# Optimization experiments

Hardware: AMD Instinct MI355X
Metric: run time of the kernel (lower is better)

The kernel has to match this reference:

```python
import jax, jax.numpy as jnp
import numpy as np

B, S, HID = 2, 1024, 2048
HQ, HKV, HD = 32, 8, 64
ROPE_BASE = 10000.0

def _rope_tables(seq_len, head_dim):
    inv_freq = 1.0 / (ROPE_BASE ** (np.arange(0, head_dim, 2, dtype=np.float32) / head_dim))
    t = np.arange(seq_len, dtype=np.float32)
    freqs = np.outer(t, inv_freq)                      # [S, d/2]
    emb = np.concatenate([freqs, freqs], axis=-1)      # [S, d]
    return jnp.asarray(np.cos(emb)), jnp.asarray(np.sin(emb))

def setup_inputs() -> dict:
    key = jax.random.key(0)
    ks = jax.random.split(key, 5)
    cos, sin = _rope_tables(S, HD)
    return {
        'hidden_states': jax.random.normal(ks[0], (B, S, HID), jnp.float32),
        'cos': cos, 'sin': sin,
        'Wq': jax.random.normal(ks[1], (HID, HID), jnp.float32) * (HID ** -0.5),
        'Wk': jax.random.normal(ks[2], (HID, HKV * HD), jnp.float32) * (HID ** -0.5),
        'Wv': jax.random.normal(ks[3], (HID, HKV * HD), jnp.float32) * (HID ** -0.5),
        'Wo': jax.random.normal(ks[4], (HID, HID), jnp.float32) * (HID ** -0.5),
    }

def _rotate_half(x):
    d = x.shape[-1]
    return jnp.concatenate([-x[..., d // 2:], x[..., :d // 2]], axis=-1)

def reference(hidden_states, cos, sin, Wq, Wk, Wv, Wo):
    b, s, _ = hidden_states.shape
    q = (hidden_states @ Wq).reshape(b, s, HQ, HD)    # [b,s,Hq,d]
    k = (hidden_states @ Wk).reshape(b, s, HKV, HD)   # [b,s,Hkv,d]
    v = (hidden_states @ Wv).reshape(b, s, HKV, HD)
    # RoPE: cos/sin [s,d] broadcast as [s,1,d] over head dim
    c = cos[:, None, :]
    sn = sin[:, None, :]
    q = q * c + _rotate_half(q) * sn
    k = k * c + _rotate_half(k) * sn
    # GQA: expand kv heads to query heads (repeat_kv)
    n_rep = HQ // HKV
    k = jnp.repeat(k, n_rep, axis=2)                  # [b,s,Hq,d]
    v = jnp.repeat(v, n_rep, axis=2)
    scale = HD ** -0.5
    scores = jnp.einsum('bqhd,bkhd->bhqk', q, k) * scale  # [b,Hq,s,s]
    causal = jnp.tril(jnp.ones((s, s), bool))
    scores = jnp.where(causal, scores, jnp.float32(-1e30))
    probs = jax.nn.softmax(scores.astype(jnp.float32), axis=-1).astype(q.dtype)
    out = jnp.einsum('bhqk,bkhd->bqhd', probs, v).reshape(b, s, HID)
    return out @ Wo
```

## Files before the change

### kernel.cpp

```cpp
#include <hip/hip_runtime.h>
#include <math.h>

#define B_   2
#define S_   1024
#define HID_ 2048
#define HQ_  32
#define HKV_ 8
#define HD_  64
#define NQKV 3072

#define PCHUNK 2097152

using short8  = __attribute__((ext_vector_type(8))) short;
using floatx4 = __attribute__((ext_vector_type(4))) float;

__device__ __forceinline__ unsigned short f2bf(float x) {
    unsigned int u = __builtin_bit_cast(unsigned int, x);
    u += 0x7FFFu + ((u >> 16) & 1u);
    return (unsigned short)(u >> 16);
}
__device__ __forceinline__ float bf2f(unsigned short u) {
    return __builtin_bit_cast(float, (unsigned int)u << 16);
}

__device__ __forceinline__ void gl_lds16(const unsigned short* g, unsigned short* l) {
    __builtin_amdgcn_global_load_lds(
        (const __attribute__((address_space(1))) void*)g,
        (__attribute__((address_space(3))) void*)l, 16, 0, 0);
}

__global__ __launch_bounds__(256) void gemm_qkv(const unsigned short* __restrict__ A,
                                                const unsigned short* __restrict__ Bt,
                                                unsigned short* __restrict__ Qp,
                                                unsigned short* __restrict__ KVp) {
    __shared__ __align__(16) unsigned short As[128 * 64];
    __shared__ __align__(16) unsigned short Bs[128 * 64];

    int bid = blockIdx.x;
    int m0, n0, z, Nw, nc0;
    unsigned short* C;
    if (bid < 512) {
        n0 = (bid & 15) * 128; m0 = ((bid >> 4) & 15) * 128; z = bid >> 8;
        C = Qp + (size_t)z * 2048 * 2048; Nw = 2048; nc0 = n0;
    } else {
        bid -= 512;
        n0 = 2048 + (bid & 7) * 128; m0 = ((bid >> 3) & 15) * 128; z = bid >> 7;
        C = KVp + (size_t)z * 2048 * 1024; Nw = 1024; nc0 = n0 - 2048;
    }
    const int kbase = z * 1024;

    const int tid  = threadIdx.x;
    const int w    = tid >> 6;
    const int lane = tid & 63;
    const int col  = lane & 15;
    const int quad = lane >> 4;
    const int wm = (w >> 1) * 64;
    const int wn = (w & 1) * 64;

    const int srow = lane >> 3;
    const int scol = ((lane & 7) ^ srow) * 8;
    const unsigned short* Ag = A  + (size_t)(m0 + w * 32 + srow) * HID_ + scol;
    const unsigned short* Bg = Bt + (size_t)(n0 + w * 32 + srow) * HID_ + scol;

    floatx4 acc[4][4] = {};

    for (int k0 = kbase; k0 < kbase + 1024; k0 += 64) {
#pragma unroll
        for (int c = 0; c < 4; ++c) {
            gl_lds16(Ag + (size_t)(8 * c) * HID_ + k0, &As[(w * 32 + 8 * c) * 64]);
            gl_lds16(Bg + (size_t)(8 * c) * HID_ + k0, &Bs[(w * 32 + 8 * c) * 64]);
        }
        __syncthreads();

#pragma unroll
        for (int hh = 0; hh < 2; ++hh) {
            short8 af[4], bfr[4];
#pragma unroll
            for (int i = 0; i < 4; ++i)
                af[i] = *(const short8*)&As[(wm + i * 16 + col) * 64
                                            + (((hh * 4 + quad) ^ (col & 7)) << 3)];
#pragma unroll
            for (int j = 0; j < 4; ++j)
                bfr[j] = *(const short8*)&Bs[(wn + j * 16 + col) * 64
                                             + (((hh * 4 + quad) ^ (col & 7)) << 3)];
#pragma unroll
            for (int i = 0; i < 4; ++i)
#pragma unroll
                for (int j = 0; j < 4; ++j)
                    acc[i][j] = __builtin_amdgcn_mfma_f32_16x16x32_bf16(
                        af[i], bfr[j], acc[i][j], 0, 0, 0);
        }
        __syncthreads();
    }

#pragma unroll
    for (int i = 0; i < 4; ++i)
#pragma unroll
        for (int j = 0; j < 4; ++j)
#pragma unroll
            for (int r = 0; r < 4; ++r)
                C[(size_t)(m0 + wm + i * 16 + quad * 4 + r) * Nw
                  + (nc0 + wn + j * 16 + col)] = f2bf(acc[i][j][r]);
}

__global__ __launch_bounds__(256) void gemm_wo(const unsigned short* __restrict__ A,
                                               const unsigned short* __restrict__ Bt,
                                               float* __restrict__ Cf,
                                               unsigned short* __restrict__ Cp1) {
    __shared__ __align__(16) unsigned short As[128 * 64];
    __shared__ __align__(16) unsigned short Bs[128 * 64];

    const int m0 = blockIdx.y * 128;
    const int n0 = blockIdx.x * 128;
    const int z  = blockIdx.z;
    const int kbase = z * 1024;

    const int tid  = threadIdx.x;
    const int w    = tid >> 6;
    const int lane = tid & 63;
    const int col  = lane & 15;
    const int quad = lane >> 4;
    const int wm = (w >> 1) * 64;
    const int wn = (w & 1) * 64;

    const int srow = lane >> 3;
    const int scol = ((lane & 7) ^ srow) * 8;
    const unsigned short* Ag = A  + (size_t)(m0 + w * 32 + srow) * HID_ + scol;
    const unsigned short* Bg = Bt + (size_t)(n0 + w * 32 + srow) * HID_ + scol;

    floatx4 acc[4][4] = {};

    for (int k0 = kbase; k0 < kbase + 1024; k0 += 64) {
#pragma unroll
        for (int c = 0; c < 4; ++c) {
            gl_lds16(Ag + (size_t)(8 * c) * HID_ + k0, &As[(w * 32 + 8 * c) * 64]);
            gl_lds16(Bg + (size_t)(8 * c) * HID_ + k0, &Bs[(w * 32 + 8 * c) * 64]);
        }
        __syncthreads();

#pragma unroll
        for (int hh = 0; hh < 2; ++hh) {
            short8 af[4], bfr[4];
#pragma unroll
            for (int i = 0; i < 4; ++i)
                af[i] = *(const short8*)&As[(wm + i * 16 + col) * 64
                                            + (((hh * 4 + quad) ^ (col & 7)) << 3)];
#pragma unroll
            for (int j = 0; j < 4; ++j)
                bfr[j] = *(const short8*)&Bs[(wn + j * 16 + col) * 64
                                             + (((hh * 4 + quad) ^ (col & 7)) << 3)];
#pragma unroll
            for (int i = 0; i < 4; ++i)
#pragma unroll
                for (int j = 0; j < 4; ++j)
                    acc[i][j] = __builtin_amdgcn_mfma_f32_16x16x32_bf16(
                        af[i], bfr[j], acc[i][j], 0, 0, 0);
        }
        __syncthreads();
    }

#pragma unroll
    for (int i = 0; i < 4; ++i)
#pragma unroll
        for (int j = 0; j < 4; ++j)
#pragma unroll
            for (int r = 0; r < 4; ++r) {
                size_t off = (size_t)(m0 + wm + i * 16 + quad * 4 + r) * HID_
                           + (n0 + wn + j * 16 + col);
                if (z == 0) Cf[off] = acc[i][j][r];
                else        Cp1[off] = f2bf(acc[i][j][r]);
            }
}

__global__ __launch_bounds__(256) void reduce_wo(float* __restrict__ out,
                                                 const unsigned short* __restrict__ p1) {
    int i4 = (blockIdx.x * 256 + threadIdx.x) * 4;
    float4 o = *(float4*)&out[i4];
    ushort4 p = *(const ushort4*)&p1[i4];
    o.x += bf2f(p.x); o.y += bf2f(p.y); o.z += bf2f(p.z); o.w += bf2f(p.w);
    *(float4*)&out[i4] = o;
}

__global__ __launch_bounds__(256) void prep(const float* __restrict__ X,
                                            const float* __restrict__ Wq,
                                            const float* __restrict__ Wk,
                                            const float* __restrict__ Wv,
                                            const float* __restrict__ Wo,
                                            unsigned short* __restrict__ Xbf,
                                            unsigned short* __restrict__ WcatT,
                                            unsigned short* __restrict__ WoT) {
    __shared__ float tile[32][33];
    int bid = blockIdx.x;
    if (bid < 4096) {
        int tid = bid * 256 + threadIdx.x;
        float4 v = *(const float4*)&X[(size_t)tid * 4];
        ushort4 o = {f2bf(v.x), f2bf(v.y), f2bf(v.z), f2bf(v.w)};
        *(ushort4*)&Xbf[(size_t)tid * 4] = o;
        return;
    }
    const float* W;
    unsigned short* WT;
    int N, tn0, tk0;
    if (bid < 10240) {
        bid -= 4096;
        if (bid < 4096) {
            W = Wq; WT = WcatT; N = HID_;
            tn0 = (bid & 63) * 32; tk0 = (bid >> 6) * 32;
        } else if (bid < 5120) {
            bid -= 4096;
            W = Wk; WT = WcatT + (size_t)HID_ * HID_; N = 512;
            tn0 = (bid & 15) * 32; tk0 = (bid >> 4) * 32;
        } else {
            bid -= 5120;
            W = Wv; WT = WcatT + (size_t)(HID_ + 512) * HID_; N = 512;
            tn0 = (bid & 15) * 32; tk0 = (bid >> 4) * 32;
        }
    } else {
        bid -= 10240;
        W = Wo; WT = WoT; N = HID_;
        tn0 = (bid & 63) * 32; tk0 = (bid >> 6) * 32;
    }
    const int r  = threadIdx.x >> 3;
    const int c4 = (threadIdx.x & 7) * 4;
    float4 v = *(const float4*)&W[(size_t)(tk0 + r) * N + tn0 + c4];
    tile[r][c4 + 0] = v.x;
    tile[r][c4 + 1] = v.y;
    tile[r][c4 + 2] = v.z;
    tile[r][c4 + 3] = v.w;
    __syncthreads();
    ushort4 o = {f2bf(tile[c4 + 0][r]), f2bf(tile[c4 + 1][r]),
                 f2bf(tile[c4 + 2][r]), f2bf(tile[c4 + 3][r])};
    *(ushort4*)&WT[(size_t)(tn0 + r) * HID_ + tk0 + c4] = o;
}

__global__ __launch_bounds__(256) void transpose_wo(const float* __restrict__ Wo,
                                                    unsigned short* __restrict__ WoT) {
    __shared__ float tile[32][33];
    int bid = blockIdx.x;
    const int tn0 = (bid & 63) * 32;
    const int tk0 = (bid >> 6) * 32;
    const int r  = threadIdx.x >> 3;
    const int c4 = (threadIdx.x & 7) * 4;
    float4 v = *(const float4*)&Wo[(size_t)(tk0 + r) * HID_ + tn0 + c4];
    tile[r][c4 + 0] = v.x;
    tile[r][c4 + 1] = v.y;
    tile[r][c4 + 2] = v.z;
    tile[r][c4 + 3] = v.w;
    __syncthreads();
    ushort4 o = {f2bf(tile[c4 + 0][r]), f2bf(tile[c4 + 1][r]),
                 f2bf(tile[c4 + 2][r]), f2bf(tile[c4 + 3][r])};
    *(ushort4*)&WoT[(size_t)(tn0 + r) * HID_ + tk0 + c4] = o;
}

__global__ __launch_bounds__(256) void convert_qkv(const unsigned short* __restrict__ Qp,
                                                   const unsigned short* __restrict__ KVp,
                                                   const float* __restrict__ cosT,
                                                   const float* __restrict__ sinT,
                                                   unsigned short* __restrict__ Qbf,
                                                   unsigned short* __restrict__ Kbf,
                                                   unsigned short* __restrict__ Vt) {
    const size_t QSTR  = (size_t)2048 * 2048;
    const size_t KVSTR = (size_t)2048 * 1024;
    int tid = blockIdx.x * 256 + threadIdx.x;
    const int NQ4 = 524288;
    const int NK4 = 131072;
    if (tid < NQ4) {
        int d0 = (tid & 7) * 4;
        int h  = (tid >> 3) & 31;
        int s  = (tid >> 8) & 1023;
        int b  = tid >> 18;
        const unsigned short* row = Qp + (size_t)(b * S_ + s) * 2048 + h * HD_;
        ushort4 a0 = *(const ushort4*)&row[d0];
        ushort4 a1 = *(const ushort4*)&row[d0 + 32];
        ushort4 p0 = *(const ushort4*)&row[QSTR + d0];
        ushort4 p1 = *(const ushort4*)&row[QSTR + d0 + 32];
        float4 c0  = *(const float4*)&cosT[s * HD_ + d0];
        float4 sn0 = *(const float4*)&sinT[s * HD_ + d0];
        float4 c1  = *(const float4*)&cosT[s * HD_ + d0 + 32];
        float4 sn1 = *(const float4*)&sinT[s * HD_ + d0 + 32];
        ushort4 o0, o1;
#pragma unroll
        for (int j = 0; j < 4; ++j) {
            float x0 = bf2f(((const unsigned short*)&a0)[j]) +
                       bf2f(((const unsigned short*)&p0)[j]);
            float x1 = bf2f(((const unsigned short*)&a1)[j]) +
                       bf2f(((const unsigned short*)&p1)[j]);
            ((unsigned short*)&o0)[j] =
                f2bf((x0 * ((const float*)&c0)[j] - x1 * ((const float*)&sn0)[j]) * 0.125f);
            ((unsigned short*)&o1)[j] =
                f2bf((x1 * ((const float*)&c1)[j] + x0 * ((const float*)&sn1)[j]) * 0.125f);
        }
        unsigned short* orow = Qbf + ((size_t)(b * HQ_ + h) * S_ + s) * HD_;
        *(ushort4*)&orow[d0]      = o0;
        *(ushort4*)&orow[d0 + 32] = o1;
    } else if (tid < NQ4 + NK4) {
        tid -= NQ4;
        int d0 = (tid & 7) * 4;
        int kv = (tid >> 3) & 7;
        int s  = (tid >> 6) & 1023;
        int b  = tid >> 16;
        const unsigned short* row = KVp + (size_t)(b * S_ + s) * 1024 + kv * HD_;
        ushort4 a0 = *(const ushort4*)&row[d0];
        ushort4 a1 = *(const ushort4*)&row[d0 + 32];
        ushort4 p0 = *(const ushort4*)&row[KVSTR + d0];
        ushort4 p1 = *(const ushort4*)&row[KVSTR + d0 + 32];
        float4 c0  = *(const float4*)&cosT[s * HD_ + d0];
        float4 sn0 = *(const float4*)&sinT[s * HD_ + d0];
        float4 c1  = *(const float4*)&cosT[s * HD_ + d0 + 32];
        float4 sn1 = *(const float4*)&sinT[s * HD_ + d0 + 32];
        ushort4 o0, o1;
#pragma unroll
        for (int j = 0; j < 4; ++j) {
            float x0 = bf2f(((const unsigned short*)&a0)[j]) +
                       bf2f(((const unsigned short*)&p0)[j]);
            float x1 = bf2f(((const unsigned short*)&a1)[j]) +
                       bf2f(((const unsigned short*)&p1)[j]);
            ((unsigned short*)&o0)[j] =
                f2bf(x0 * ((const float*)&c0)[j] - x1 * ((const float*)&sn0)[j]);
            ((unsigned short*)&o1)[j] =
                f2bf(x1 * ((const float*)&c1)[j] + x0 * ((const float*)&sn1)[j]);
        }
        unsigned short* orow = Kbf + ((size_t)(b * HKV_ + kv) * S_ + s) * HD_;
        *(ushort4*)&orow[d0]      = o0;
        *(ushort4*)&orow[d0 + 32] = o1;
    } else {
        tid -= NQ4 + NK4;
        int s4 = tid & 255;
        int d  = (tid >> 8) & (HD_ - 1);
        int kv = (tid >> 14) & (HKV_ - 1);
        int b  = tid >> 17;
        int s  = s4 * 4;
        const unsigned short* base =
            KVp + ((size_t)(b * S_ + s)) * 1024 + 512 + kv * HD_ + d;
        ushort4 o;
#pragma unroll
        for (int j = 0; j < 4; ++j) {
            float v = bf2f(base[(size_t)j * 1024]) +
                      bf2f(base[KVSTR + (size_t)j * 1024]);
            ((unsigned short*)&o)[j] = f2bf(v);
        }
        *(ushort4*)&Vt[((size_t)(b * HKV_ + kv) * HD_ + d) * S_ + s] = o;
    }
}

__global__ __launch_bounds__(256) void attn_mfma(const unsigned short* __restrict__ Qbf,
                                                 const unsigned short* __restrict__ Kbf,
                                                 const unsigned short* __restrict__ Vt,
                                                 unsigned short* __restrict__ Ctx,
                                                 float* __restrict__ PO,
                                                 float* __restrict__ ML) {
    const int x  = blockIdx.x;
    const int kv = blockIdx.y;
    const int b  = blockIdx.z;

    int tq, chunk, it0, it1;
    if (x < 32) {
        tq = 16 + (x >> 1); chunk = x & 1;
        const int ns = (32 * tq + 95) >> 6;
        const int hh = ns >> 1;
        it0 = chunk ? hh : 0;
        it1 = chunk ? ns : hh;
    } else {
        tq = 47 - x; chunk = -1;
        it0 = 0;
        it1 = (32 * tq + 95) >> 6;
    }

    const int w    = threadIdx.x >> 6;
    const int lane = threadIdx.x & 63;
    const int col  = lane & 15;
    const int quad = lane >> 4;

    const int h   = kv * 4 + w;
    const int bh  = b * HQ_ + h;
    const int bkv = b * HKV_ + kv;
    const int qw  = 32 * tq;

    __shared__ __align__(16) unsigned short sK[2][64 * 64];
    __shared__ __align__(16) unsigned short sV[2][64 * 64];
    __shared__ __align__(16) unsigned short sP[4][16 * 64];
    unsigned short* myP = sP[w];

    short8 bq[2][2];
#pragma unroll
    for (int u = 0; u < 2; ++u) {
        const unsigned short* qrow = Qbf + ((size_t)bh * S_ + qw + 16 * u + col) * HD_;
        bq[u][0] = *(const short8*)&qrow[quad * 8];
        bq[u][1] = *(const short8*)&qrow[32 + quad * 8];
    }

    const unsigned short* Kbase = Kbf + (size_t)bkv * S_ * HD_;
    const unsigned short* Vbase = Vt  + (size_t)bkv * HD_ * S_;

    const int sr  = lane >> 3;
    const int ssl = (lane & 7) ^ sr;
    const int r0  = 16 * w;

    floatx4 acc[2][4] = {};
    float m_i[2] = {-1e30f, -1e30f};
    float l_i[2] = {0.f, 0.f};

    {
        const int kb = it0 * 64;
#pragma unroll
        for (int c = 0; c < 2; ++c) {
            const int row = r0 + 8 * c + sr;
            gl_lds16(Kbase + (size_t)(kb + row) * HD_ + ssl * 8, &sK[0][(r0 + 8 * c) * 64]);
            gl_lds16(Vbase + (size_t)row * S_ + kb + ssl * 8,    &sV[0][(r0 + 8 * c) * 64]);
        }
    }
    __syncthreads();

    int cur = 0;
    for (int it = it0; it < it1; ++it) {
        const int k0 = it * 64;

        if (it + 1 < it1) {
            const int kn = k0 + 64;
#pragma unroll
            for (int c = 0; c < 2; ++c) {
                const int row = r0 + 8 * c + sr;
                gl_lds16(Kbase + (size_t)(kn + row) * HD_ + ssl * 8,
                         &sK[cur ^ 1][(r0 + 8 * c) * 64]);
                gl_lds16(Vbase + (size_t)row * S_ + kn + ssl * 8,
                         &sV[cur ^ 1][(r0 + 8 * c) * 64]);
            }
        }

        floatx4 sc[2][4];
        __builtin_amdgcn_s_setprio(1);
#pragma unroll
        for (int tt = 0; tt < 4; ++tt) {
            const int krow = 16 * tt + col;
            const unsigned short* kr = &sK[cur][krow * 64];
            short8 ak0 = *(const short8*)&kr[((quad    ) ^ (krow & 7)) * 8];
            short8 ak1 = *(const short8*)&kr[((quad + 4) ^ (krow & 7)) * 8];
#pragma unroll
            for (int u = 0; u < 2; ++u) {
                floatx4 z = {0.f, 0.f, 0.f, 0.f};
                z = __builtin_amdgcn_mfma_f32_16x16x32_bf16(ak0, bq[u][0], z, 0, 0, 0);
                z = __builtin_amdgcn_mfma_f32_16x16x32_bf16(ak1, bq[u][1], z, 0, 0, 0);
                sc[u][tt] = z;
            }
        }
        __builtin_amdgcn_s_setprio(0);

        short8 pa[2][2];
#pragma unroll
        for (int u = 0; u < 2; ++u) {
            const int qbase = qw + 16 * u;
            const int myq   = qbase + col;
            if (k0 + 63 > qbase) {
#pragma unroll
                for (int tt = 0; tt < 4; ++tt)
#pragma unroll
                    for (int r = 0; r < 4; ++r)
                        if (k0 + 16 * tt + quad * 4 + r > myq) sc[u][tt][r] = -1e30f;
            }
            float vmax = sc[u][0][0];
#pragma unroll
            for (int tt = 0; tt < 4; ++tt)
#pragma unroll
                for (int r = 0; r < 4; ++r)
                    vmax = fmaxf(vmax, sc[u][tt][r]);
            vmax = fmaxf(vmax, __shfl_xor(vmax, 16, 64));
            vmax = fmaxf(vmax, __shfl_xor(vmax, 32, 64));

            if (!__all(vmax <= m_i[u] + 8.0f)) {
                const float mnew  = fmaxf(m_i[u], vmax);
                const float alpha = __expf(m_i[u] - mnew);
                m_i[u] = mnew;
                l_i[u] *= alpha;
#pragma unroll
                for (int nt = 0; nt < 4; ++nt)
#pragma unroll
                    for (int r = 0; r < 4; ++r)
                        acc[u][nt][r] *= alpha;
            }
            const float mu = m_i[u];

            float lsum = 0.f;
#pragma unroll
            for (int tt = 0; tt < 4; ++tt) {
                float p0 = __expf(sc[u][tt][0] - mu);
                float p1 = __expf(sc[u][tt][1] - mu);
                float p2 = __expf(sc[u][tt][2] - mu);
                float p3 = __expf(sc[u][tt][3] - mu);
                lsum += (p0 + p1) + (p2 + p3);
                ushort4 pk = {f2bf(p0), f2bf(p1), f2bf(p2), f2bf(p3)};
                *(ushort4*)&myP[col * 64
                                + ((((4 * tt + quad) >> 1) ^ (col & 7)) << 3)
                                + (quad & 1) * 4] = pk;
            }
            lsum += __shfl_xor(lsum, 16, 64);
            lsum += __shfl_xor(lsum, 32, 64);
            l_i[u] += lsum;

            pa[u][0] = *(const short8*)&myP[col * 64 + (((quad    ) ^ (col & 7)) << 3)];
            pa[u][1] = *(const short8*)&myP[col * 64 + (((4 + quad) ^ (col & 7)) << 3)];
        }

        __builtin_amdgcn_s_setprio(1);
#pragma unroll
        for (int nt = 0; nt < 4; ++nt) {
            const int vrow = 16 * nt + col;
            const unsigned short* vr = &sV[cur][vrow * 64];
            short8 vb0 = *(const short8*)&vr[((quad    ) ^ (vrow & 7)) * 8];
            short8 vb1 = *(const short8*)&vr[((quad + 4) ^ (vrow & 7)) * 8];
#pragma unroll
            for (int u = 0; u < 2; ++u) {
                acc[u][nt] = __builtin_amdgcn_mfma_f32_16x16x32_bf16(vb0, pa[u][0], acc[u][nt], 0, 0, 0);
                acc[u][nt] = __builtin_amdgcn_mfma_f32_16x16x32_bf16(vb1, pa[u][1], acc[u][nt], 0, 0, 0);
            }
        }
        __builtin_amdgcn_s_setprio(0);

        __syncthreads();
        cur ^= 1;
    }

    if (chunk < 0) {
#pragma unroll
        for (int u = 0; u < 2; ++u) {
            const float invl = 1.0f / l_i[u];
            unsigned short* crow =
                Ctx + (size_t)(b * S_ + qw + 16 * u + col) * HID_ + h * HD_;
#pragma unroll
            for (int nt = 0; nt < 4; ++nt) {
                ushort4 o = {f2bf(acc[u][nt][0] * invl), f2bf(acc[u][nt][1] * invl),
                             f2bf(acc[u][nt][2] * invl), f2bf(acc[u][nt][3] * invl)};
                *(ushort4*)&crow[nt * 16 + quad * 4] = o;
            }
        }
    } else {
        const int ts = tq - 16;
        const int base_row = (((b * 8 + kv) * 16 + ts) * 4 + w) * 32;
        float* POc = PO + (size_t)chunk * PCHUNK;
#pragma unroll
        for (int u = 0; u < 2; ++u) {
            float* prow = &POc[(size_t)(base_row + 16 * u + col) * 64];
#pragma unroll
            for (int nt = 0; nt < 4; ++nt)
                *(floatx4*)&prow[nt * 16 + quad * 4] = acc[u][nt];
            if (quad == 0) {
                const int rr = chunk * 32768 + base_row + 16 * u + col;
                ML[rr * 2 + 0] = m_i[u];
                ML[rr * 2 + 1] = l_i[u];
            }
        }
    }
}

__global__ __launch_bounds__(256) void merge_attn(const float* __restrict__ PO,
                                                  const float* __restrict__ ML,
                                                  unsigned short* __restrict__ Ctx) {
    const int tid = blockIdx.x * 256 + threadIdx.x;
    const int i4  = tid * 4;
    const int row = i4 >> 6;
    const int d0  = i4 & 63;

    const float m0 = ML[row * 2 + 0];
    const float l0 = ML[row * 2 + 1];
    const float m1 = ML[(32768 + row) * 2 + 0];
    const float l1 = ML[(32768 + row) * 2 + 1];
    const float mf = fmaxf(m0, m1);
    const float s0 = __expf(m0 - mf);
    const float s1 = __expf(m1 - mf);
    const float inv = 1.0f / (l0 * s0 + l1 * s1);

    float4 o0 = *(const float4*)&PO[(size_t)row * 64 + d0];
    float4 o1 = *(const float4*)&PO[(size_t)PCHUNK + (size_t)row * 64 + d0];

    const int q  = row & 31;
    const int hh = (row >> 5) & 3;
    const int ts = (row >> 7) & 15;
    const int kv = (row >> 11) & 7;
    const int b  = row >> 14;
    const int q_abs = 512 + ts * 32 + q;
    const int h_abs = kv * 4 + hh;

    ushort4 o;
    o.x = f2bf((o0.x * s0 + o1.x * s1) * inv);
    o.y = f2bf((o0.y * s0 + o1.y * s1) * inv);
    o.z = f2bf((o0.z * s0 + o1.z * s1) * inv);
    o.w = f2bf((o0.w * s0 + o1.w * s1) * inv);
    *(ushort4*)&Ctx[((size_t)(b * S_ + q_abs)) * HID_ + h_abs * HD_ + d0] = o;
}

extern "C" void kernel_launch(void* const* d_in, const int* in_sizes, int n_in,
                              void* d_out, int out_size, void* d_ws, size_t ws_size,
                              hipStream_t stream) {
    const float* X    = (const float*)d_in[0];
    const float* cosT = (const float*)d_in[1];
    const float* sinT = (const float*)d_in[2];
    const float* Wq   = (const float*)d_in[3];
    const float* Wk   = (const float*)d_in[4];
    const float* Wv   = (const float*)d_in[5];
    const float* Wo   = (const float*)d_in[6];

    const int M = B_ * S_;
    const size_t MB = 1024u * 1024u;

    char* ws = (char*)d_ws;
    const bool bigws = ws_size >= 40 * MB;

    unsigned short* Xbf   = (unsigned short*)(ws);
    unsigned short* Qbf   = (unsigned short*)(ws);
    unsigned short* WcatT = (unsigned short*)(ws + 8 * MB);
    unsigned short* Kbf   = (unsigned short*)(ws + 8 * MB);
    unsigned short* Vt    = (unsigned short*)(ws + 10 * MB);
    unsigned short* WoT   = (unsigned short*)(ws + (bigws ? 28 : 12) * MB);
    float*          MLb   = (float*)(ws + (bigws ? 36 : 12) * MB);
    unsigned short* KVp   = (unsigned short*)(ws + 20 * MB);
    unsigned short* Ctxbf = (unsigned short*)(ws + 20 * MB);
    unsigned short* Wop1  = (unsigned short*)(ws);
    unsigned short* Qp    = (unsigned short*)d_out;
    float*          PO    = (float*)d_out;
    float* out = (float*)d_out;

    prep<<<bigws ? 14336 : 10240, 256, 0, stream>>>(X, Wq, Wk, Wv, Wo,
                                                    Xbf, WcatT, WoT);

    gemm_qkv<<<768, 256, 0, stream>>>(Xbf, WcatT, Qp, KVp);

    convert_qkv<<<3584, 256, 0, stream>>>(Qp, KVp, cosT, sinT, Qbf, Kbf, Vt);

    attn_mfma<<<dim3(48, HKV_, B_), 256, 0, stream>>>(Qbf, Kbf, Vt, Ctxbf,
                                                      PO, MLb);

    merge_attn<<<2048, 256, 0, stream>>>(PO, MLb, Ctxbf);

    if (!bigws)
        transpose_wo<<<4096, 256, 0, stream>>>(Wo, WoT);

    gemm_wo<<<dim3(16, 16, 2), 256, 0, stream>>>(Ctxbf, WoT, out, Wop1);

    reduce_wo<<<(M * HID_ / 4) / 256, 256, 0, stream>>>(out, Wop1);
}
```

Baseline: 229.2 us.

## Fuse Q RoPE into attention, use exp2 softmax, and swizzle GEMM block order

The bigws path stops materialising a rotated Q tensor: attention now loads the split-K partial Q sums, adds them, and applies RoPE and scaling in registers, so convert_qkv only handles K and V. Q is prescaled by log2(e), which lets softmax and the merge step use exp2f. Both GEMMs remap block indices with an XCD-style interleave to improve L2 locality. The bigws threshold rises to 64MB with a new workspace layout, so smaller workspaces fall back to the old path, and each Q row is now rotated redundantly in the attention blocks that read it.

```diff
diff --git a/kernel.cpp b/kernel.cpp
--- a/kernel.cpp
+++ b/kernel.cpp
@@ -10,6 +10,7 @@
 #define NQKV 3072
 
 #define PCHUNK 2097152
+#define QSC   (0.125f * 1.44269504089f)
 
 using short8  = __attribute__((ext_vector_type(8))) short;
 using floatx4 = __attribute__((ext_vector_type(4))) float;
@@ -36,7 +37,7 @@
     __shared__ __align__(16) unsigned short As[128 * 64];
     __shared__ __align__(16) unsigned short Bs[128 * 64];
 
-    int bid = blockIdx.x;
+    int bid = (blockIdx.x & 7) * 96 + (blockIdx.x >> 3);
     int m0, n0, z, Nw, nc0;
     unsigned short* C;
     if (bid < 512) {
@@ -110,9 +111,10 @@
     __shared__ __align__(16) unsigned short As[128 * 64];
     __shared__ __align__(16) unsigned short Bs[128 * 64];
 
-    const int m0 = blockIdx.y * 128;
-    const int n0 = blockIdx.x * 128;
-    const int z  = blockIdx.z;
+    int bid = (blockIdx.x & 7) * 64 + (blockIdx.x >> 3);
+    const int z  = bid >> 8;
+    const int m0 = ((bid >> 4) & 15) * 128;
+    const int n0 = (bid & 15) * 128;
     const int kbase = z * 1024;
 
     const int tid  = threadIdx.x;
@@ -258,43 +260,48 @@
                                                    const float* __restrict__ sinT,
                                                    unsigned short* __restrict__ Qbf,
                                                    unsigned short* __restrict__ Kbf,
-                                                   unsigned short* __restrict__ Vt) {
+                                                   unsigned short* __restrict__ Vt,
+                                                   int withQ) {
     const size_t QSTR  = (size_t)2048 * 2048;
     const size_t KVSTR = (size_t)2048 * 1024;
     int tid = blockIdx.x * 256 + threadIdx.x;
     const int NQ4 = 524288;
     const int NK4 = 131072;
-    if (tid < NQ4) {
-        int d0 = (tid & 7) * 4;
-        int h  = (tid >> 3) & 31;
-        int s  = (tid >> 8) & 1023;
-        int b  = tid >> 18;
-        const unsigned short* row = Qp + (size_t)(b * S_ + s) * 2048 + h * HD_;
-        ushort4 a0 = *(const ushort4*)&row[d0];
-        ushort4 a1 = *(const ushort4*)&row[d0 + 32];
-        ushort4 p0 = *(const ushort4*)&row[QSTR + d0];
-        ushort4 p1 = *(const ushort4*)&row[QSTR + d0 + 32];
-        float4 c0  = *(const float4*)&cosT[s * HD_ + d0];
-        float4 sn0 = *(const float4*)&sinT[s * HD_ + d0];
-        float4 c1  = *(const float4*)&cosT[s * HD_ + d0 + 32];
-        float4 sn1 = *(const float4*)&sinT[s * HD_ + d0 + 32];
-        ushort4 o0, o1;
-#pragma unroll
-        for (int j = 0; j < 4; ++j) {
-            float x0 = bf2f(((const unsigned short*)&a0)[j]) +
-                       bf2f(((const unsigned short*)&p0)[j]);
-            float x1 = bf2f(((const unsigned short*)&a1)[j]) +
-                       bf2f(((const unsigned short*)&p1)[j]);
-            ((unsigned short*)&o0)[j] =
-                f2bf((x0 * ((const float*)&c0)[j] - x1 * ((const float*)&sn0)[j]) * 0.125f);
-            ((unsigned short*)&o1)[j] =
-                f2bf((x1 * ((const float*)&c1)[j] + x0 * ((const float*)&sn1)[j]) * 0.125f);
-        }
-        unsigned short* orow = Qbf + ((size_t)(b * HQ_ + h) * S_ + s) * HD_;
-        *(ushort4*)&orow[d0]      = o0;
-        *(ushort4*)&orow[d0 + 32] = o1;
-    } else if (tid < NQ4 + NK4) {
+    if (withQ) {
+        if (tid < NQ4) {
+            int d0 = (tid & 7) * 4;
+            int h  = (tid >> 3) & 31;
+            int s  = (tid >> 8) & 1023;
+            int b  = tid >> 18;
+            const unsigned short* row = Qp + (size_t)(b * S_ + s) * 2048 + h * HD_;
+            ushort4 a0 = *(const ushort4*)&row[d0];
+            ushort4 a1 = *(const ushort4*)&row[d0 + 32];
+            ushort4 p0 = *(const ushort4*)&row[QSTR + d0];
+            ushort4 p1 = *(const ushort4*)&row[QSTR + d0 + 32];
+            float4 c0  = *(const float4*)&cosT[s * HD_ + d0];
+            float4 sn0 = *(const float4*)&sinT[s * HD_ + d0];
+            float4 c1  = *(const float4*)&cosT[s * HD_ + d0 + 32];
+            float4 sn1 = *(const float4*)&sinT[s * HD_ + d0 + 32];
+            ushort4 o0, o1;
+#pragma unroll
+            for (int j = 0; j < 4; ++j) {
+                float x0 = bf2f(((const unsigned short*)&a0)[j]) +
+                           bf2f(((const unsigned short*)&p0)[j]);
+                float x1 = bf2f(((const unsigned short*)&a1)[j]) +
+                           bf2f(((const unsigned short*)&p1)[j]);
+                ((unsigned short*)&o0)[j] =
+                    f2bf((x0 * ((const float*)&c0)[j] - x1 * ((const float*)&sn0)[j]) * QSC);
+                ((unsigned short*)&o1)[j] =
+                    f2bf((x1 * ((const float*)&c1)[j] + x0 * ((const float*)&sn1)[j]) * QSC);
+            }
+            unsigned short* orow = Qbf + ((size_t)(b * HQ_ + h) * S_ + s) * HD_;
+            *(ushort4*)&orow[d0]      = o0;
+            *(ushort4*)&orow[d0 + 32] = o1;
+            return;
+        }
         tid -= NQ4;
+    }
+    if (tid < NK4) {
         int d0 = (tid & 7) * 4;
         int kv = (tid >> 3) & 7;
         int s  = (tid >> 6) & 1023;
@@ -324,7 +331,7 @@
         *(ushort4*)&orow[d0]      = o0;
         *(ushort4*)&orow[d0 + 32] = o1;
     } else {
-        tid -= NQ4 + NK4;
+        tid -= NK4;
         int s4 = tid & 255;
         int d  = (tid >> 8) & (HD_ - 1);
         int kv = (tid >> 14) & (HKV_ - 1);
@@ -343,12 +350,15 @@
     }
 }
 
-__global__ __launch_bounds__(256) void attn_mfma(const unsigned short* __restrict__ Qbf,
+__global__ __launch_bounds__(256) void attn_mfma(const unsigned short* __restrict__ Qsrc,
                                                  const unsigned short* __restrict__ Kbf,
                                                  const unsigned short* __restrict__ Vt,
+                                                 const float* __restrict__ cosT,
+                                                 const float* __restrict__ sinT,
                                                  unsigned short* __restrict__ Ctx,
                                                  float* __restrict__ PO,
-                                                 float* __restrict__ ML) {
+                                                 float* __restrict__ ML,
+                                                 int qdirect) {
     const int x  = blockIdx.x;
     const int kv = blockIdx.y;
     const int b  = blockIdx.z;
@@ -382,11 +392,47 @@
     unsigned short* myP = sP[w];
 
     short8 bq[2][2];
-#pragma unroll
-    for (int u = 0; u < 2; ++u) {
-        const unsigned short* qrow = Qbf + ((size_t)bh * S_ + qw + 16 * u + col) * HD_;
-        bq[u][0] = *(const short8*)&qrow[quad * 8];
-        bq[u][1] = *(const short8*)&qrow[32 + quad * 8];
+    if (qdirect) {
+        const size_t QSTR = (size_t)2048 * 2048;
+        const int d8 = quad * 8;
+#pragma unroll
+        for (int u = 0; u < 2; ++u) {
+            const int s = qw + 16 * u + col;
+            const unsigned short* row = Qsrc + (size_t)(b * S_ + s) * 2048 + h * HD_;
+            short8 a0 = *(const short8*)&row[d8];
+            short8 a1 = *(const short8*)&row[d8 + 32];
+            short8 p0 = *(const short8*)&row[QSTR + d8];
+            short8 p1 = *(const short8*)&row[QSTR + d8 + 32];
+            float4 c0a  = *(const float4*)&cosT[s * HD_ + d8];
+            float4 c0b  = *(const float4*)&cosT[s * HD_ + d8 + 4];
+            float4 sn0a = *(const float4*)&sinT[s * HD_ + d8];
+            float4 sn0b = *(const float4*)&sinT[s * HD_ + d8 + 4];
+            float4 c1a  = *(const float4*)&cosT[s * HD_ + d8 + 32];
+            float4 c1b  = *(const float4*)&cosT[s * HD_ + d8 + 36];
+            float4 sn1a = *(const float4*)&sinT[s * HD_ + d8 + 32];
+            float4 sn1b = *(const float4*)&sinT[s * HD_ + d8 + 36];
+            short8 q0, q1;
+#pragma unroll
+            for (int j = 0; j < 8; ++j) {
+                float x0 = bf2f((unsigned short)a0[j]) + bf2f((unsigned short)p0[j]);
+                float x1 = bf2f((unsigned short)a1[j]) + bf2f((unsigned short)p1[j]);
+                float cj0 = (j < 4 ? ((const float*)&c0a)[j]  : ((const float*)&c0b)[j - 4]);
+                float sj0 = (j < 4 ? ((const float*)&sn0a)[j] : ((const float*)&sn0b)[j - 4]);
+                float cj1 = (j < 4 ? ((const float*)&c1a)[j]  : ((const float*)&c1b)[j - 4]);
+                float sj1 = (j < 4 ? ((const float*)&sn1a)[j] : ((const float*)&sn1b)[j - 4]);
+                q0[j] = (short)f2bf((x0 * cj0 - x1 * sj0) * QSC);
+                q1[j] = (short)f2bf((x1 * cj1 + x0 * sj1) * QSC);
+            }
+            bq[u][0] = q0;
+            bq[u][1] = q1;
+        }
+    } else {
+#pragma unroll
+        for (int u = 0; u < 2; ++u) {
+            const unsigned short* qrow = Qsrc + ((size_t)bh * S_ + qw + 16 * u + col) * HD_;
+            bq[u][0] = *(const short8*)&qrow[quad * 8];
+            bq[u][1] = *(const short8*)&qrow[32 + quad * 8];
+        }
     }
 
     const unsigned short* Kbase = Kbf + (size_t)bkv * S_ * HD_;
@@ -468,7 +514,7 @@
 
             if (!__all(vmax <= m_i[u] + 8.0f)) {
                 const float mnew  = fmaxf(m_i[u], vmax);
-                const float alpha = __expf(m_i[u] - mnew);
+                const float alpha = exp2f(m_i[u] - mnew);
                 m_i[u] = mnew;
                 l_i[u] *= alpha;
 #pragma unroll
@@ -482,10 +528,10 @@
             float lsum = 0.f;
 #pragma unroll
             for (int tt = 0; tt < 4; ++tt) {
-                float p0 = __expf(sc[u][tt][0] - mu);
-                float p1 = __expf(sc[u][tt][1] - mu);
-                float p2 = __expf(sc[u][tt][2] - mu);
-                float p3 = __expf(sc[u][tt][3] - mu);
+                float p0 = exp2f(sc[u][tt][0] - mu);
+                float p1 = exp2f(sc[u][tt][1] - mu);
+                float p2 = exp2f(sc[u][tt][2] - mu);
+                float p3 = exp2f(sc[u][tt][3] - mu);
                 lsum += (p0 + p1) + (p2 + p3);
                 ushort4 pk = {f2bf(p0), f2bf(p1), f2bf(p2), f2bf(p3)};
                 *(ushort4*)&myP[col * 64
@@ -564,8 +610,8 @@
     const float m1 = ML[(32768 + row) * 2 + 0];
     const float l1 = ML[(32768 + row) * 2 + 1];
     const float mf = fmaxf(m0, m1);
-    const float s0 = __expf(m0 - mf);
-    const float s1 = __expf(m1 - mf);
+    const float s0 = exp2f(m0 - mf);
+    const float s1 = exp2f(m1 - mf);
     const float inv = 1.0f / (l0 * s0 + l1 * s1);
 
     float4 o0 = *(const float4*)&PO[(size_t)row * 64 + d0];
@@ -602,38 +648,54 @@
     const size_t MB = 1024u * 1024u;
 
     char* ws = (char*)d_ws;
-    const bool bigws = ws_size >= 40 * MB;
-
-    unsigned short* Xbf   = (unsigned short*)(ws);
-    unsigned short* Qbf   = (unsigned short*)(ws);
-    unsigned short* WcatT = (unsigned short*)(ws + 8 * MB);
-    unsigned short* Kbf   = (unsigned short*)(ws + 8 * MB);
-    unsigned short* Vt    = (unsigned short*)(ws + 10 * MB);
-    unsigned short* WoT   = (unsigned short*)(ws + (bigws ? 28 : 12) * MB);
-    float*          MLb   = (float*)(ws + (bigws ? 36 : 12) * MB);
-    unsigned short* KVp   = (unsigned short*)(ws + 20 * MB);
-    unsigned short* Ctxbf = (unsigned short*)(ws + 20 * MB);
-    unsigned short* Wop1  = (unsigned short*)(ws);
-    unsigned short* Qp    = (unsigned short*)d_out;
-    float*          PO    = (float*)d_out;
-    float* out = (float*)d_out;
-
-    prep<<<bigws ? 14336 : 10240, 256, 0, stream>>>(X, Wq, Wk, Wv, Wo,
-                                                    Xbf, WcatT, WoT);
-
-    gemm_qkv<<<768, 256, 0, stream>>>(Xbf, WcatT, Qp, KVp);
-
-    convert_qkv<<<3584, 256, 0, stream>>>(Qp, KVp, cosT, sinT, Qbf, Kbf, Vt);
-
-    attn_mfma<<<dim3(48, HKV_, B_), 256, 0, stream>>>(Qbf, Kbf, Vt, Ctxbf,
-                                                      PO, MLb);
-
-    merge_attn<<<2048, 256, 0, stream>>>(PO, MLb, Ctxbf);
-
-    if (!bigws)
+    const bool bigws = ws_size >= 64 * MB;
+
+    if (bigws) {
+        unsigned short* Xbf   = (unsigned short*)(ws);
+        unsigned short* WcatT = (unsigned short*)(ws + 8 * MB);
+        unsigned short* Kbf   = (unsigned short*)(ws + 8 * MB);
+        unsigned short* Vt    = (unsigned short*)(ws + 10 * MB);
+        unsigned short* KVp   = (unsigned short*)(ws + 20 * MB);
+        unsigned short* Ctxbf = (unsigned short*)(ws + 20 * MB);
+        unsigned short* Qp    = (unsigned short*)(ws + 28 * MB);
+        float*          MLb   = (float*)(ws + 45 * MB);
+        unsigned short* WoT   = (unsigned short*)(ws + 48 * MB);
+        unsigned short* Wop1  = (unsigned short*)(ws);
+        float*          PO    = (float*)d_out;
+        float* out = (float*)d_out;
+
+        prep<<<14336, 256, 0, stream>>>(X, Wq, Wk, Wv, Wo, Xbf, WcatT, WoT);
+        gemm_qkv<<<768, 256, 0, stream>>>(Xbf, WcatT, Qp, KVp);
+        convert_qkv<<<1536, 256, 0, stream>>>(Qp, KVp, cosT, sinT,
+                                              (unsigned short*)nullptr, Kbf, Vt, 0);
+        attn_mfma<<<dim3(48, HKV_, B_), 256, 0, stream>>>(Qp, Kbf, Vt, cosT, sinT,
+                                                          Ctxbf, PO, MLb, 1);
+        merge_attn<<<2048, 256, 0, stream>>>(PO, MLb, Ctxbf);
+        gemm_wo<<<512, 256, 0, stream>>>(Ctxbf, WoT, out, Wop1);
+        reduce_wo<<<(M * HID_ / 4) / 256, 256, 0, stream>>>(out, Wop1);
+    } else {
+        unsigned short* Xbf   = (unsigned short*)(ws);
+        unsigned short* Qbf   = (unsigned short*)(ws);
+        unsigned short* WcatT = (unsigned short*)(ws + 8 * MB);
+        unsigned short* Kbf   = (unsigned short*)(ws + 8 * MB);
+        unsigned short* Vt    = (unsigned short*)(ws + 10 * MB);
+        unsigned short* WoT   = (unsigned short*)(ws + 12 * MB);
+        float*          MLb   = (float*)(ws + 12 * MB);
+        unsigned short* KVp   = (unsigned short*)(ws + 20 * MB);
+        unsigned short* Ctxbf = (unsigned short*)(ws + 20 * MB);
+        unsigned short* Wop1  = (unsigned short*)(ws);
+        unsigned short* Qp    = (unsigned short*)d_out;
+        float*          PO    = (float*)d_out;
+        float* out = (float*)d_out;
+
+        prep<<<10240, 256, 0, stream>>>(X, Wq, Wk, Wv, Wo, Xbf, WcatT, WoT);
+        gemm_qkv<<<768, 256, 0, stream>>>(Xbf, WcatT, Qp, KVp);
+        convert_qkv<<<3584, 256, 0, stream>>>(Qp, KVp, cosT, sinT, Qbf, Kbf, Vt, 1);
+        attn_mfma<<<dim3(48, HKV_, B_), 256, 0, stream>>>(Qbf, Kbf, Vt, cosT, sinT,
+                                                          Ctxbf, PO, MLb, 0);
+        merge_attn<<<2048, 256, 0, stream>>>(PO, MLb, Ctxbf);
         transpose_wo<<<4096, 256, 0, stream>>>(Wo, WoT);
-
-    gemm_wo<<<dim3(16, 16, 2), 256, 0, stream>>>(Ctxbf, WoT, out, Wop1);
-
-    reduce_wo<<<(M * HID_ / 4) / 256, 256, 0, stream>>>(out, Wop1);
-}
+        gemm_wo<<<512, 256, 0, stream>>>(Ctxbf, WoT, out, Wop1);
+        reduce_wo<<<(M * HID_ / 4) / 256, 256, 0, stream>>>(out, Wop1);
+    }
+}
```

New measurement: 225.8 us. About the same (-1.5%).
